# Optimization experiments

Hardware: AMD Instinct MI355X
Metric: run time of the kernel (lower is better)

The kernel has to match this reference:

```python
import jax, jax.numpy as jnp
import numpy as np

N = 4  # hypercomplex dimension

def setup_inputs() -> dict:
    key = jax.random.key(0)
    k1, k2, k3 = jax.random.split(key, 3)
    x = jax.random.normal(k1, (32, 196, 768), dtype=jnp.float32)
    # [n, out_pad/n, in_pad/n] = [4, 3072//4, 768//4]
    weight_components = jax.random.normal(k2, (N, 768, 192), dtype=jnp.float32) * 0.02
    bias = jax.random.normal(k3, (3072,), dtype=jnp.float32) * 0.02
    return {"x": x, "weight_components": weight_components, "bias": bias}

def reference(x, weight_components, bias):
    n, out_blk, in_blk = weight_components.shape
    batch_shape = x.shape[:-1]
    xb = x.reshape(-1, n, in_blk)  # [B, n, in_blk]
    # original: out[:, (i+j)%n] += x[:, j] @ W[i].T
    # equivalently out[:, k] = sum_j x[:, j] @ W[(k-j)%n].T
    k_idx = jnp.arange(n)[:, None]
    j_idx = jnp.arange(n)[None, :]
    Wperm = weight_components[(k_idx - j_idx) % n]  # [n(k), n(j), out_blk, in_blk]
    out = jnp.einsum('bjc,kjoc->bko', xb, Wperm)    # [B, n, out_blk]
    out = out.reshape(-1, n * out_blk) + bias
    return out.reshape(*batch_shape, n * out_blk)
```

## Files before the change

### kernel.cpp

```cpp
#include <hip/hip_runtime.h>
#include <stdint.h>

#define M_ROWS 6272
#define K_DIM  768
#define N_DIM  3072
#define BM 128
#define BN 128
#define BK 32
#define NITER (K_DIM / BK)

#define X_CHUNKS (M_ROWS * K_DIM / 8)
#define W_CHUNKS (N_DIM * K_DIM / 8)
#define X_BLOCKS (X_CHUNKS / 256)
#define W_BLOCKS (W_CHUNKS / 256)

typedef unsigned short u16;
typedef __attribute__((ext_vector_type(8))) __bf16 bf16x8;
typedef __attribute__((ext_vector_type(4))) float f32x4;

__device__ __forceinline__ u16 f32_to_bf16(float f) {
    unsigned u = __float_as_uint(f);
    unsigned r = 0x7FFFu + ((u >> 16) & 1u);
    return (u16)((u + r) >> 16);
}

__device__ __forceinline__ unsigned pack2(float a, float b) {
    return (unsigned)f32_to_bf16(a) | ((unsigned)f32_to_bf16(b) << 16);
}

__device__ __forceinline__ void lds_barrier() {
    asm volatile("s_waitcnt lgkmcnt(0)\n\ts_barrier" ::: "memory");
}

__global__ void prep_kernel(const float* __restrict__ x, const float* __restrict__ w,
                            u16* __restrict__ xb, u16* __restrict__ wb) {
    int b = blockIdx.x;
    if (b < X_BLOCKS) {
        int idx = b * 256 + threadIdx.x;
        const float4* xp = (const float4*)x + (size_t)idx * 2;
        float4 a = xp[0], c = xp[1];
        uint4 v;
        v.x = pack2(a.x, a.y);
        v.y = pack2(a.z, a.w);
        v.z = pack2(c.x, c.y);
        v.w = pack2(c.z, c.w);
        ((uint4*)xb)[idx] = v;
    } else {
        int idx = (b - X_BLOCKS) * 256 + threadIdx.x;
        int n    = idx / 96;
        int kc   = idx - n * 96;
        int kblk = n / 768;
        int o    = n - kblk * 768;
        int j    = kc / 24;
        int c8   = kc - j * 24;
        int i    = (kblk - j) & 3;
        const float* src = w + (((size_t)i * 768 + o) * 192 + c8 * 8);
        float4 a = ((const float4*)src)[0];
        float4 c = ((const float4*)src)[1];
        uint4 v;
        v.x = pack2(a.x, a.y);
        v.y = pack2(a.z, a.w);
        v.z = pack2(c.x, c.y);
        v.w = pack2(c.z, c.w);
        ((uint4*)wb)[idx] = v;
    }
}

__global__ __launch_bounds__(256) void gemm_bt(
    const u16* __restrict__ A,
    const u16* __restrict__ B,
    const float* __restrict__ bias,
    float* __restrict__ C)
{
    __shared__ u16 As[2][BM * BK];
    __shared__ u16 Bs[2][BN * BK];

    const int tid    = threadIdx.x;
    const int wave   = tid >> 6;
    const int lane   = tid & 63;
    const int lane16 = lane & 15;
    const int quad   = lane >> 4;
    const int wr     = wave >> 1;
    const int wc     = wave & 1;

    const int rowBase = blockIdx.y * BM;
    const int colBase = blockIdx.x * BN;

    const int c0 = tid;
    const int c1 = tid + 256;
    const int r0 = c0 >> 2, s0 = (c0 & 3) ^ ((r0 >> 1) & 3);
    const int r1 = c1 >> 2, s1 = (c1 & 3) ^ ((r1 >> 1) & 3);
    const uint4* Ag0 = (const uint4*)(A + (size_t)(rowBase + r0) * K_DIM + s0 * 8);
    const uint4* Ag1 = (const uint4*)(A + (size_t)(rowBase + r1) * K_DIM + s1 * 8);
    const uint4* Bg0 = (const uint4*)(B + (size_t)(colBase + r0) * K_DIM + s0 * 8);
    const uint4* Bg1 = (const uint4*)(B + (size_t)(colBase + r1) * K_DIM + s1 * 8);
    uint4* Al0 = (uint4*)&As[0][c0 * 8];
    uint4* Al1 = (uint4*)&As[0][c1 * 8];
    uint4* Bl0 = (uint4*)&Bs[0][c0 * 8];
    uint4* Bl1 = (uint4*)&Bs[0][c1 * 8];
    const int bufStride = (BM * BK) / 8;

    const int swz  = (lane16 >> 1) & 3;
    const int slot = (quad ^ swz) * 8;
    int aoff[4], boff[4];
#pragma unroll
    for (int i = 0; i < 4; ++i)
        aoff[i] = (wr * 64 + i * 16 + lane16) * BK + slot;
#pragma unroll
    for (int j = 0; j < 4; ++j)
        boff[j] = (wc * 64 + j * 16 + lane16) * BK + slot;

    f32x4 acc[4][4] = {};

    const int kStep = BK / 8;

    uint4 ga0 = Ag0[0], ga1 = Ag1[0], gb0 = Bg0[0], gb1 = Bg1[0];
    Al0[0] = ga0; Al1[0] = ga1; Bl0[0] = gb0; Bl1[0] = gb1;
    ga0 = Ag0[kStep]; ga1 = Ag1[kStep]; gb0 = Bg0[kStep]; gb1 = Bg1[kStep];
    lds_barrier();

#pragma unroll 2
    for (int it = 0; it < NITER - 2; ++it) {
        const int cur = it & 1, nxt = cur ^ 1;

        bf16x8 af[4], bfv[4];
#pragma unroll
        for (int i = 0; i < 4; ++i)
            af[i] = *(const bf16x8*)&As[cur][aoff[i]];
#pragma unroll
        for (int j = 0; j < 4; ++j)
            bfv[j] = *(const bf16x8*)&Bs[cur][boff[j]];
#pragma unroll
        for (int i = 0; i < 4; ++i)
#pragma unroll
            for (int j = 0; j < 4; ++j)
                acc[i][j] = __builtin_amdgcn_mfma_f32_16x16x32_bf16(
                    af[i], bfv[j], acc[i][j], 0, 0, 0);

        const int o = nxt * bufStride;
        Al0[o] = ga0; Al1[o] = ga1; Bl0[o] = gb0; Bl1[o] = gb1;
        const int g = (it + 2) * kStep;
        ga0 = Ag0[g]; ga1 = Ag1[g]; gb0 = Bg0[g]; gb1 = Bg1[g];
        lds_barrier();
    }

    {
        const int cur = (NITER - 2) & 1, nxt = cur ^ 1;
        bf16x8 af[4], bfv[4];
#pragma unroll
        for (int i = 0; i < 4; ++i)
            af[i] = *(const bf16x8*)&As[cur][aoff[i]];
#pragma unroll
        for (int j = 0; j < 4; ++j)
            bfv[j] = *(const bf16x8*)&Bs[cur][boff[j]];
#pragma unroll
        for (int i = 0; i < 4; ++i)
#pragma unroll
            for (int j = 0; j < 4; ++j)
                acc[i][j] = __builtin_amdgcn_mfma_f32_16x16x32_bf16(
                    af[i], bfv[j], acc[i][j], 0, 0, 0);
        const int o = nxt * bufStride;
        Al0[o] = ga0; Al1[o] = ga1; Bl0[o] = gb0; Bl1[o] = gb1;
        lds_barrier();
    }

    {
        const int cur = (NITER - 1) & 1;
        bf16x8 af[4], bfv[4];
#pragma unroll
        for (int i = 0; i < 4; ++i)
            af[i] = *(const bf16x8*)&As[cur][aoff[i]];
#pragma unroll
        for (int j = 0; j < 4; ++j)
            bfv[j] = *(const bf16x8*)&Bs[cur][boff[j]];
#pragma unroll
        for (int i = 0; i < 4; ++i)
#pragma unroll
            for (int j = 0; j < 4; ++j)
                acc[i][j] = __builtin_amdgcn_mfma_f32_16x16x32_bf16(
                    af[i], bfv[j], acc[i][j], 0, 0, 0);
    }

    float bv[4];
#pragma unroll
    for (int j = 0; j < 4; ++j)
        bv[j] = bias[colBase + wc * 64 + j * 16 + lane16];
#pragma unroll
    for (int i = 0; i < 4; ++i) {
        int row0 = rowBase + wr * 64 + i * 16 + quad * 4;
#pragma unroll
        for (int r = 0; r < 4; ++r) {
            float* cp = C + (size_t)(row0 + r) * N_DIM + colBase + wc * 64 + lane16;
#pragma unroll
            for (int j = 0; j < 4; ++j)
                cp[j * 16] = acc[i][j][r] + bv[j];
        }
    }
}

extern "C" void kernel_launch(void* const* d_in, const int* in_sizes, int n_in,
                              void* d_out, int out_size, void* d_ws, size_t ws_size,
                              hipStream_t stream) {
    const float* x    = (const float*)d_in[0];
    const float* w    = (const float*)d_in[1];
    const float* bias = (const float*)d_in[2];
    float* out = (float*)d_out;

    u16* xb = (u16*)d_ws;
    u16* wb = (u16*)((char*)d_ws + (size_t)M_ROWS * K_DIM * 2);

    hipLaunchKernelGGL(prep_kernel, dim3(X_BLOCKS + W_BLOCKS), dim3(256),
                       0, stream, x, w, xb, wb);
    hipLaunchKernelGGL(gemm_bt, dim3(N_DIM / BN, M_ROWS / BM), dim3(256),
                       0, stream, xb, wb, bias, out);
}
```

Measured before the change: 134.4 us.

## Load A fragments directly from global into registers, bypassing LDS

The A operand tile is no longer staged through shared memory. Each wave loads its own MFMA A fragments straight from global memory into registers, prefetching one K-step ahead, while B stays in double-buffered LDS. This removes the A LDS writes and reads and halves LDS usage, which may allow more resident blocks. In exchange, the two waves that share a row group (wc=0 and wc=1) now each fetch the same A data from global memory, relying on L1/L2 for reuse. Each lane's 16-byte loads also follow a strided-row pattern that coalesces less well.

```diff
diff --git a/kernel.cpp b/kernel.cpp
--- a/kernel.cpp
+++ b/kernel.cpp
@@ -72,7 +72,6 @@
     const float* __restrict__ bias,
     float* __restrict__ C)
 {
-    __shared__ u16 As[2][BM * BK];
     __shared__ u16 Bs[2][BN * BK];
 
     const int tid    = threadIdx.x;
@@ -83,50 +82,53 @@
     const int wr     = wave >> 1;
     const int wc     = wave & 1;
 
-    const int rowBase = blockIdx.y * BM;
+    const int rowBase = blockIdx.y * BM + wr * 64;
     const int colBase = blockIdx.x * BN;
+
+    const u16* ap[4];
+#pragma unroll
+    for (int i = 0; i < 4; ++i)
+        ap[i] = A + (size_t)(rowBase + i * 16 + lane16) * K_DIM + quad * 8;
 
     const int c0 = tid;
     const int c1 = tid + 256;
     const int r0 = c0 >> 2, s0 = (c0 & 3) ^ ((r0 >> 1) & 3);
     const int r1 = c1 >> 2, s1 = (c1 & 3) ^ ((r1 >> 1) & 3);
-    const uint4* Ag0 = (const uint4*)(A + (size_t)(rowBase + r0) * K_DIM + s0 * 8);
-    const uint4* Ag1 = (const uint4*)(A + (size_t)(rowBase + r1) * K_DIM + s1 * 8);
     const uint4* Bg0 = (const uint4*)(B + (size_t)(colBase + r0) * K_DIM + s0 * 8);
     const uint4* Bg1 = (const uint4*)(B + (size_t)(colBase + r1) * K_DIM + s1 * 8);
-    uint4* Al0 = (uint4*)&As[0][c0 * 8];
-    uint4* Al1 = (uint4*)&As[0][c1 * 8];
     uint4* Bl0 = (uint4*)&Bs[0][c0 * 8];
     uint4* Bl1 = (uint4*)&Bs[0][c1 * 8];
-    const int bufStride = (BM * BK) / 8;
+    const int bufStride = (BN * BK) / 8;
+    const int kStep = BK / 8;
 
     const int swz  = (lane16 >> 1) & 3;
     const int slot = (quad ^ swz) * 8;
-    int aoff[4], boff[4];
-#pragma unroll
-    for (int i = 0; i < 4; ++i)
-        aoff[i] = (wr * 64 + i * 16 + lane16) * BK + slot;
+    int boff[4];
 #pragma unroll
     for (int j = 0; j < 4; ++j)
         boff[j] = (wc * 64 + j * 16 + lane16) * BK + slot;
 
     f32x4 acc[4][4] = {};
 
-    const int kStep = BK / 8;
-
-    uint4 ga0 = Ag0[0], ga1 = Ag1[0], gb0 = Bg0[0], gb1 = Bg1[0];
-    Al0[0] = ga0; Al1[0] = ga1; Bl0[0] = gb0; Bl1[0] = gb1;
-    ga0 = Ag0[kStep]; ga1 = Ag1[kStep]; gb0 = Bg0[kStep]; gb1 = Bg1[kStep];
+    uint4 gb0 = Bg0[0], gb1 = Bg1[0];
+    Bl0[0] = gb0; Bl1[0] = gb1;
+    gb0 = Bg0[kStep]; gb1 = Bg1[kStep];
+    bf16x8 a0[4], a1[4];
+#pragma unroll
+    for (int i = 0; i < 4; ++i) a0[i] = *(const bf16x8*)(ap[i]);
     lds_barrier();
 
 #pragma unroll 2
     for (int it = 0; it < NITER - 2; ++it) {
         const int cur = it & 1, nxt = cur ^ 1;
 
-        bf16x8 af[4], bfv[4];
-#pragma unroll
-        for (int i = 0; i < 4; ++i)
-            af[i] = *(const bf16x8*)&As[cur][aoff[i]];
+        {
+            const int k = (it + 1) * BK;
+#pragma unroll
+            for (int i = 0; i < 4; ++i) a1[i] = *(const bf16x8*)(ap[i] + k);
+        }
+
+        bf16x8 bfv[4];
 #pragma unroll
         for (int j = 0; j < 4; ++j)
             bfv[j] = *(const bf16x8*)&Bs[cur][boff[j]];
@@ -135,21 +137,25 @@
 #pragma unroll
             for (int j = 0; j < 4; ++j)
                 acc[i][j] = __builtin_amdgcn_mfma_f32_16x16x32_bf16(
-                    af[i], bfv[j], acc[i][j], 0, 0, 0);
+                    a0[i], bfv[j], acc[i][j], 0, 0, 0);
 
         const int o = nxt * bufStride;
-        Al0[o] = ga0; Al1[o] = ga1; Bl0[o] = gb0; Bl1[o] = gb1;
+        Bl0[o] = gb0; Bl1[o] = gb1;
         const int g = (it + 2) * kStep;
-        ga0 = Ag0[g]; ga1 = Ag1[g]; gb0 = Bg0[g]; gb1 = Bg1[g];
+        gb0 = Bg0[g]; gb1 = Bg1[g];
+#pragma unroll
+        for (int i = 0; i < 4; ++i) a0[i] = a1[i];
         lds_barrier();
     }
 
     {
         const int cur = (NITER - 2) & 1, nxt = cur ^ 1;
-        bf16x8 af[4], bfv[4];
-#pragma unroll
-        for (int i = 0; i < 4; ++i)
-            af[i] = *(const bf16x8*)&As[cur][aoff[i]];
+        {
+            const int k = (NITER - 1) * BK;
+#pragma unroll
+            for (int i = 0; i < 4; ++i) a1[i] = *(const bf16x8*)(ap[i] + k);
+        }
+        bf16x8 bfv[4];
 #pragma unroll
         for (int j = 0; j < 4; ++j)
             bfv[j] = *(const bf16x8*)&Bs[cur][boff[j]];
@@ -158,18 +164,17 @@
 #pragma unroll
             for (int j = 0; j < 4; ++j)
                 acc[i][j] = __builtin_amdgcn_mfma_f32_16x16x32_bf16(
-                    af[i], bfv[j], acc[i][j], 0, 0, 0);
+                    a0[i], bfv[j], acc[i][j], 0, 0, 0);
         const int o = nxt * bufStride;
-        Al0[o] = ga0; Al1[o] = ga1; Bl0[o] = gb0; Bl1[o] = gb1;
+        Bl0[o] = gb0; Bl1[o] = gb1;
+#pragma unroll
+        for (int i = 0; i < 4; ++i) a0[i] = a1[i];
         lds_barrier();
     }
 
     {
         const int cur = (NITER - 1) & 1;
-        bf16x8 af[4], bfv[4];
-#pragma unroll
-        for (int i = 0; i < 4; ++i)
-            af[i] = *(const bf16x8*)&As[cur][aoff[i]];
+        bf16x8 bfv[4];
 #pragma unroll
         for (int j = 0; j < 4; ++j)
             bfv[j] = *(const bf16x8*)&Bs[cur][boff[j]];
@@ -178,7 +183,7 @@
 #pragma unroll
             for (int j = 0; j < 4; ++j)
                 acc[i][j] = __builtin_amdgcn_mfma_f32_16x16x32_bf16(
-                    af[i], bfv[j], acc[i][j], 0, 0, 0);
+                    a0[i], bfv[j], acc[i][j], 0, 0, 0);
     }
 
     float bv[4];
@@ -187,7 +192,7 @@
         bv[j] = bias[colBase + wc * 64 + j * 16 + lane16];
 #pragma unroll
     for (int i = 0; i < 4; ++i) {
-        int row0 = rowBase + wr * 64 + i * 16 + quad * 4;
+        int row0 = rowBase + i * 16 + quad * 4;
 #pragma unroll
         for (int r = 0; r < 4; ++r) {
             float* cp = C + (size_t)(row0 + r) * N_DIM + colBase + wc * 64 + lane16;
```

Result: slower. 159.0 us (+18.3%).

## Deepen GEMM pipeline with four LDS stages and register double-buffered fragments

Applied to the files above, without the earlier changes.

Replaces the two-stage LDS double buffer with a four-buffer ring and prefetches the next iteration's MFMA operand fragments into registers before issuing the current MFMAs. Global loads run two tiles ahead and LDS writes target a buffer not being read, so LDS reads, global loads and MFMAs can overlap within one barrier interval. The loop is fully unrolled. This raises LDS use to 64 KB per block and adds fragment registers, which may reduce occupancy or cause spills.

```diff
diff --git a/kernel.cpp b/kernel.cpp
--- a/kernel.cpp
+++ b/kernel.cpp
@@ -72,8 +72,8 @@
     const float* __restrict__ bias,
     float* __restrict__ C)
 {
-    __shared__ u16 As[2][BM * BK];
-    __shared__ u16 Bs[2][BN * BK];
+    __shared__ u16 As[4][BM * BK];
+    __shared__ u16 Bs[4][BN * BK];
 
     const int tid    = threadIdx.x;
     const int wave   = tid >> 6;
@@ -94,11 +94,9 @@
     const uint4* Ag1 = (const uint4*)(A + (size_t)(rowBase + r1) * K_DIM + s1 * 8);
     const uint4* Bg0 = (const uint4*)(B + (size_t)(colBase + r0) * K_DIM + s0 * 8);
     const uint4* Bg1 = (const uint4*)(B + (size_t)(colBase + r1) * K_DIM + s1 * 8);
-    uint4* Al0 = (uint4*)&As[0][c0 * 8];
-    uint4* Al1 = (uint4*)&As[0][c1 * 8];
-    uint4* Bl0 = (uint4*)&Bs[0][c0 * 8];
-    uint4* Bl1 = (uint4*)&Bs[0][c1 * 8];
-    const int bufStride = (BM * BK) / 8;
+    const int l0 = c0 * 8;
+    const int l1 = c1 * 8;
+    const int kStep = BK / 8;
 
     const int swz  = (lane16 >> 1) & 3;
     const int slot = (quad ^ swz) * 8;
@@ -112,73 +110,89 @@
 
     f32x4 acc[4][4] = {};
 
-    const int kStep = BK / 8;
-
-    uint4 ga0 = Ag0[0], ga1 = Ag1[0], gb0 = Bg0[0], gb1 = Bg1[0];
-    Al0[0] = ga0; Al1[0] = ga1; Bl0[0] = gb0; Bl1[0] = gb1;
-    ga0 = Ag0[kStep]; ga1 = Ag1[kStep]; gb0 = Bg0[kStep]; gb1 = Bg1[kStep];
+    uint4 gA0[2], gA1[2], gB0[2], gB1[2];
+    bf16x8 afr[2][4], bfr[2][4];
+
+    gA0[0] = Ag0[0]; gA1[0] = Ag1[0]; gB0[0] = Bg0[0]; gB1[0] = Bg1[0];
+    *(uint4*)&As[0][l0] = gA0[0]; *(uint4*)&As[0][l1] = gA1[0];
+    *(uint4*)&Bs[0][l0] = gB0[0]; *(uint4*)&Bs[0][l1] = gB1[0];
+    gA0[1] = Ag0[kStep]; gA1[1] = Ag1[kStep]; gB0[1] = Bg0[kStep]; gB1[1] = Bg1[kStep];
+    *(uint4*)&As[1][l0] = gA0[1]; *(uint4*)&As[1][l1] = gA1[1];
+    *(uint4*)&Bs[1][l0] = gB0[1]; *(uint4*)&Bs[1][l1] = gB1[1];
+    gA0[0] = Ag0[2 * kStep]; gA1[0] = Ag1[2 * kStep];
+    gB0[0] = Bg0[2 * kStep]; gB1[0] = Bg1[2 * kStep];
     lds_barrier();
-
-#pragma unroll 2
-    for (int it = 0; it < NITER - 2; ++it) {
-        const int cur = it & 1, nxt = cur ^ 1;
-
-        bf16x8 af[4], bfv[4];
-#pragma unroll
-        for (int i = 0; i < 4; ++i)
-            af[i] = *(const bf16x8*)&As[cur][aoff[i]];
-#pragma unroll
-        for (int j = 0; j < 4; ++j)
-            bfv[j] = *(const bf16x8*)&Bs[cur][boff[j]];
-#pragma unroll
-        for (int i = 0; i < 4; ++i)
-#pragma unroll
-            for (int j = 0; j < 4; ++j)
-                acc[i][j] = __builtin_amdgcn_mfma_f32_16x16x32_bf16(
-                    af[i], bfv[j], acc[i][j], 0, 0, 0);
-
-        const int o = nxt * bufStride;
-        Al0[o] = ga0; Al1[o] = ga1; Bl0[o] = gb0; Bl1[o] = gb1;
-        const int g = (it + 2) * kStep;
-        ga0 = Ag0[g]; ga1 = Ag1[g]; gb0 = Bg0[g]; gb1 = Bg1[g];
+#pragma unroll
+    for (int i = 0; i < 4; ++i) afr[0][i] = *(const bf16x8*)&As[0][aoff[i]];
+#pragma unroll
+    for (int j = 0; j < 4; ++j) bfr[0][j] = *(const bf16x8*)&Bs[0][boff[j]];
+
+#pragma unroll
+    for (int t = 0; t < NITER - 3; ++t) {
+        const int s  = t & 1, sn = s ^ 1;
+        const int bN = (t + 1) & 3;
+        const int bW = (t + 2) & 3;
+
+#pragma unroll
+        for (int i = 0; i < 4; ++i) afr[sn][i] = *(const bf16x8*)&As[bN][aoff[i]];
+#pragma unroll
+        for (int j = 0; j < 4; ++j) bfr[sn][j] = *(const bf16x8*)&Bs[bN][boff[j]];
+
+        *(uint4*)&As[bW][l0] = gA0[s]; *(uint4*)&As[bW][l1] = gA1[s];
+        *(uint4*)&Bs[bW][l0] = gB0[s]; *(uint4*)&Bs[bW][l1] = gB1[s];
+
+        {
+            const int g = (t + 3) * kStep;
+            gA0[sn] = Ag0[g]; gA1[sn] = Ag1[g];
+            gB0[sn] = Bg0[g]; gB1[sn] = Bg1[g];
+        }
+
+#pragma unroll
+        for (int i = 0; i < 4; ++i)
+#pragma unroll
+            for (int j = 0; j < 4; ++j)
+                acc[i][j] = __builtin_amdgcn_mfma_f32_16x16x32_bf16(
+                    afr[s][i], bfr[s][j], acc[i][j], 0, 0, 0);
+
         lds_barrier();
     }
 
     {
-        const int cur = (NITER - 2) & 1, nxt = cur ^ 1;
-        bf16x8 af[4], bfv[4];
-#pragma unroll
-        for (int i = 0; i < 4; ++i)
-            af[i] = *(const bf16x8*)&As[cur][aoff[i]];
-#pragma unroll
-        for (int j = 0; j < 4; ++j)
-            bfv[j] = *(const bf16x8*)&Bs[cur][boff[j]];
-#pragma unroll
-        for (int i = 0; i < 4; ++i)
-#pragma unroll
-            for (int j = 0; j < 4; ++j)
-                acc[i][j] = __builtin_amdgcn_mfma_f32_16x16x32_bf16(
-                    af[i], bfv[j], acc[i][j], 0, 0, 0);
-        const int o = nxt * bufStride;
-        Al0[o] = ga0; Al1[o] = ga1; Bl0[o] = gb0; Bl1[o] = gb1;
+#pragma unroll
+        for (int i = 0; i < 4; ++i) afr[0][i] = *(const bf16x8*)&As[22 & 3][aoff[i]];
+#pragma unroll
+        for (int j = 0; j < 4; ++j) bfr[0][j] = *(const bf16x8*)&Bs[22 & 3][boff[j]];
+        *(uint4*)&As[23 & 3][l0] = gA0[1]; *(uint4*)&As[23 & 3][l1] = gA1[1];
+        *(uint4*)&Bs[23 & 3][l0] = gB0[1]; *(uint4*)&Bs[23 & 3][l1] = gB1[1];
+#pragma unroll
+        for (int i = 0; i < 4; ++i)
+#pragma unroll
+            for (int j = 0; j < 4; ++j)
+                acc[i][j] = __builtin_amdgcn_mfma_f32_16x16x32_bf16(
+                    afr[1][i], bfr[1][j], acc[i][j], 0, 0, 0);
         lds_barrier();
     }
 
     {
-        const int cur = (NITER - 1) & 1;
-        bf16x8 af[4], bfv[4];
-#pragma unroll
-        for (int i = 0; i < 4; ++i)
-            af[i] = *(const bf16x8*)&As[cur][aoff[i]];
-#pragma unroll
-        for (int j = 0; j < 4; ++j)
-            bfv[j] = *(const bf16x8*)&Bs[cur][boff[j]];
-#pragma unroll
-        for (int i = 0; i < 4; ++i)
-#pragma unroll
-            for (int j = 0; j < 4; ++j)
-                acc[i][j] = __builtin_amdgcn_mfma_f32_16x16x32_bf16(
-                    af[i], bfv[j], acc[i][j], 0, 0, 0);
+#pragma unroll
+        for (int i = 0; i < 4; ++i) afr[1][i] = *(const bf16x8*)&As[23 & 3][aoff[i]];
+#pragma unroll
+        for (int j = 0; j < 4; ++j) bfr[1][j] = *(const bf16x8*)&Bs[23 & 3][boff[j]];
+#pragma unroll
+        for (int i = 0; i < 4; ++i)
+#pragma unroll
+            for (int j = 0; j < 4; ++j)
+                acc[i][j] = __builtin_amdgcn_mfma_f32_16x16x32_bf16(
+                    afr[0][i], bfr[0][j], acc[i][j], 0, 0, 0);
+    }
+
+    {
+#pragma unroll
+        for (int i = 0; i < 4; ++i)
+#pragma unroll
+            for (int j = 0; j < 4; ++j)
+                acc[i][j] = __builtin_amdgcn_mfma_f32_16x16x32_bf16(
+                    afr[1][i], bfr[1][j], acc[i][j], 0, 0, 0);
     }
 
     float bv[4];
```

Measured after the change: 182.7 us. +35.9%, slower.
